# Performance work log

Measured on AMD Instinct MI355X. Metric: run time of the kernel, lower is better.

The kernel has to match this reference:

```python
import jax, jax.numpy as jnp
import numpy as np

VOCAB, HIDDEN, BATCH, EMB, SEQ = 512, 512, 64, 256, 1024


def _lstm_cell(x, h, c, Wih, Whh, bih, bhh):
    # PyTorch LSTMCell gate order: i, f, g, o
    gates = x @ Wih.T + bih + h @ Whh.T + bhh  # [B, 4H]
    i, f, g, o = jnp.split(gates, 4, axis=-1)
    i = jax.nn.sigmoid(i)
    f = jax.nn.sigmoid(f)
    g = jnp.tanh(g)
    o = jax.nn.sigmoid(o)
    c_new = f * c + i * g
    h_new = o * jnp.tanh(c_new)
    return h_new, c_new


def setup_inputs() -> dict:
    key = jax.random.key(0)
    ks = jax.random.split(key, 12)
    s_e = 1.0 / np.sqrt(HIDDEN)
    inp = {
        "x": jax.random.randint(ks[0], (SEQ, BATCH), 0, VOCAB, dtype=jnp.int64)
        if jax.config.jax_enable_x64 else jax.random.randint(ks[0], (SEQ, BATCH), 0, VOCAB, dtype=jnp.int32),
        "h0": jnp.zeros((BATCH, HIDDEN), jnp.float32),
        "c0": jnp.zeros((BATCH, HIDDEN), jnp.float32),
        "emb": jax.random.normal(ks[1], (VOCAB, EMB), jnp.float32),
        "Wih1": jax.random.uniform(ks[2], (4 * HIDDEN, EMB), jnp.float32, -s_e, s_e),
        "Whh1": jax.random.uniform(ks[3], (4 * HIDDEN, HIDDEN), jnp.float32, -s_e, s_e),
        "bih1": jax.random.uniform(ks[4], (4 * HIDDEN,), jnp.float32, -s_e, s_e),
        "bhh1": jax.random.uniform(ks[5], (4 * HIDDEN,), jnp.float32, -s_e, s_e),
        "Wih2": jax.random.uniform(ks[6], (4 * HIDDEN, HIDDEN), jnp.float32, -s_e, s_e),
        "Whh2": jax.random.uniform(ks[7], (4 * HIDDEN, HIDDEN), jnp.float32, -s_e, s_e),
        "bih2": jax.random.uniform(ks[8], (4 * HIDDEN,), jnp.float32, -s_e, s_e),
        "bhh2": jax.random.uniform(ks[9], (4 * HIDDEN,), jnp.float32, -s_e, s_e),
        "Wfc": jax.random.uniform(ks[10], (VOCAB, HIDDEN), jnp.float32, -s_e, s_e),
        "bfc": jax.random.uniform(ks[11], (VOCAB,), jnp.float32, -s_e, s_e),
    }
    return inp


def reference(x, h0, c0, emb, Wih1, Whh1, bih1, bhh1, Wih2, Whh2, bih2, bhh2, Wfc, bfc):
    # Embedding lookup for the whole sequence: [S, B, E]
    x_emb = emb[x]

    def step(carry, xt):
        h1, c1, h2, c2 = carry
        h1, c1 = _lstm_cell(xt, h1, c1, Wih1, Whh1, bih1, bhh1)
        h2, c2 = _lstm_cell(h1, h2, c2, Wih2, Whh2, bih2, bhh2)
        return (h1, c1, h2, c2), h2

    # Both layers start from the same (h0, c0), matching the original hc1, hc2 = (hc, hc)
    _, h2_seq = jax.lax.scan(step, (h0, c0, h0, c0), x_emb)  # [S, B, H]
    # Dropout is identity in eval mode; output projection over all timesteps at once.
    out = jnp.einsum('sbh,vh->sbv', h2_seq, Wfc) + bfc  # [S, B, V]
    return out
```

## Files before the change

kernel.cpp:

```cpp
#include <hip/hip_runtime.h>

#define SEQn   1024
#define BATCHn 64
#define EMBn   256
#define HIDn   512
#define VOCn   512

#define NL1 64
#define NL2 64
#define NFC 16
#define NBLK (NL1 + NL2 + NFC)
#define NPHASE (SEQn + 2)
#define HBUF (BATCHn * HIDn)

using f16   = _Float16;
using half8 = __attribute__((ext_vector_type(8))) _Float16;
using f32x4 = __attribute__((ext_vector_type(4))) float;
using i32x4 = __attribute__((ext_vector_type(4))) int;

#define WS_FLG 0
#define WS_H1  4096
#define WS_H2  (WS_H1 + 8 * HBUF * 2)
#define WS_P1  (WS_H2 + 8 * HBUF * 2)


__device__ __forceinline__ float sigm_(float v) { return 1.0f / (1.0f + __expf(-v)); }
__device__ __forceinline__ float tanh_(float v) { return 1.0f - 2.0f / (__expf(2.0f * v) + 1.0f); }

__device__ __forceinline__ void st_u32_sc1(f16* p, unsigned v) {
  asm volatile("global_store_dword %0, %1, off sc1" :: "v"(p), "v"(v) : "memory");
}
__device__ __forceinline__ void st_b128_sc1(f16* p, f32x4 v) {
  asm volatile("global_store_dwordx4 %0, %1, off sc1" :: "v"(p), "v"(v) : "memory");
}
__device__ __forceinline__ unsigned pack2(float a, float b) {
  f16 lo = (f16)a, hi = (f16)b;
  return (unsigned)__builtin_bit_cast(unsigned short, lo)
       | ((unsigned)__builtin_bit_cast(unsigned short, hi) << 16);
}

__device__ __forceinline__ void ld_frag16(const f16* base, half8 (&a)[16]) {
  const f16* b0 = base + 2048;
  const f16* b1 = base + 6144;
  f32x4 t0,t1,t2,t3,t4,t5,t6,t7,t8,t9,t10,t11,t12,t13,t14,t15;
  asm volatile(
    "global_load_dwordx4 %0,  %16, off offset:-4096 sc1\n\t"
    "global_load_dwordx4 %1,  %16, off offset:-3072 sc1\n\t"
    "global_load_dwordx4 %2,  %16, off offset:-2048 sc1\n\t"
    "global_load_dwordx4 %3,  %16, off offset:-1024 sc1\n\t"
    "global_load_dwordx4 %4,  %16, off sc1\n\t"
    "global_load_dwordx4 %5,  %16, off offset:1024 sc1\n\t"
    "global_load_dwordx4 %6,  %16, off offset:2048 sc1\n\t"
    "global_load_dwordx4 %7,  %16, off offset:3072 sc1\n\t"
    "global_load_dwordx4 %8,  %17, off offset:-4096 sc1\n\t"
    "global_load_dwordx4 %9,  %17, off offset:-3072 sc1\n\t"
    "global_load_dwordx4 %10, %17, off offset:-2048 sc1\n\t"
    "global_load_dwordx4 %11, %17, off offset:-1024 sc1\n\t"
    "global_load_dwordx4 %12, %17, off sc1\n\t"
    "global_load_dwordx4 %13, %17, off offset:1024 sc1\n\t"
    "global_load_dwordx4 %14, %17, off offset:2048 sc1\n\t"
    "global_load_dwordx4 %15, %17, off offset:3072 sc1\n\t"
    "s_waitcnt vmcnt(0)"
    : "=&v"(t0),"=&v"(t1),"=&v"(t2),"=&v"(t3),
      "=&v"(t4),"=&v"(t5),"=&v"(t6),"=&v"(t7),
      "=&v"(t8),"=&v"(t9),"=&v"(t10),"=&v"(t11),
      "=&v"(t12),"=&v"(t13),"=&v"(t14),"=&v"(t15)
    : "v"(b0), "v"(b1)
    : "memory");
  a[0]  = __builtin_bit_cast(half8, t0);   a[1]  = __builtin_bit_cast(half8, t1);
  a[2]  = __builtin_bit_cast(half8, t2);   a[3]  = __builtin_bit_cast(half8, t3);
  a[4]  = __builtin_bit_cast(half8, t4);   a[5]  = __builtin_bit_cast(half8, t5);
  a[6]  = __builtin_bit_cast(half8, t6);   a[7]  = __builtin_bit_cast(half8, t7);
  a[8]  = __builtin_bit_cast(half8, t8);   a[9]  = __builtin_bit_cast(half8, t9);
  a[10] = __builtin_bit_cast(half8, t10);  a[11] = __builtin_bit_cast(half8, t11);
  a[12] = __builtin_bit_cast(half8, t12);  a[13] = __builtin_bit_cast(half8, t13);
  a[14] = __builtin_bit_cast(half8, t14);  a[15] = __builtin_bit_cast(half8, t15);
}

__global__ void k_init(const float* __restrict__ h0, char* __restrict__ ws) {
  int i = blockIdx.x * 256 + threadIdx.x;
  f16* h1b = (f16*)(ws + WS_H1);
  f16* h2b = (f16*)(ws + WS_H2);
  int e = i & (HBUF - 1);
  int r = e >> 9, c = e & 511;
  float v = h0[e];
  int t = (((r >> 4) * 16 + (c >> 5)) * 4 + ((c >> 3) & 3)) * 128 + (r & 15) * 8 + (c & 7);
  int b = i & ~(HBUF - 1);
  h1b[b + t] = (f16)v;
  h2b[b + t] = (f16)v;
  if (i < 1024) ((int*)ws)[i] = 0;
}

__global__ void k_p1(const float* __restrict__ emb, const float* __restrict__ Wih1,
                     const float* __restrict__ bih1, const float* __restrict__ bhh1,
                     char* __restrict__ ws) {
  __shared__ float elds[32 * 256];
  int tid = threadIdx.x;
  int vb = blockIdx.x >> 5, gb = blockIdx.x & 31;
  for (int i = tid; i < 32 * 256; i += 256) elds[i] = emb[vb * 32 * 256 + i];
  __syncthreads();
  int gl = tid & 63, vs = tid >> 6;
  int g = gb * 64 + gl;
  float bias = bih1[g] + bhh1[g];
  float acc[8];
#pragma unroll
  for (int r = 0; r < 8; ++r) acc[r] = bias;
  const float* wrow = Wih1 + g * EMBn;
#pragma unroll 4
  for (int e = 0; e < EMBn; ++e) {
    float w = wrow[e];
#pragma unroll
    for (int r = 0; r < 8; ++r) acc[r] += elds[(vs * 8 + r) * 256 + e] * w;
  }
  f16* P1 = (f16*)(ws + WS_P1);
#pragma unroll
  for (int r = 0; r < 8; ++r) P1[(vb * 32 + vs * 8 + r) * 2048 + g] = (f16)acc[r];
}

__global__ void __launch_bounds__(256, 1)
k_lstm(const int* __restrict__ x, const float* __restrict__ c0,
       const float* __restrict__ Whh1,
       const float* __restrict__ Wih2, const float* __restrict__ Whh2,
       const float* __restrict__ bih2, const float* __restrict__ bhh2,
       const float* __restrict__ Wfc, const float* __restrict__ bfc,
       float* __restrict__ out, char* __restrict__ ws)
{
  __shared__ float part[2][64][34];
  __shared__ f16 p1s[VOCn * 32];
  __shared__ alignas(16) f16 hstage[4][16][8];

  f16* h1base = (f16*)(ws + WS_H1);
  f16* h2base = (f16*)(ws + WS_H2);
  const f16* P1 = (const f16*)(ws + WS_P1);

  const int bid = blockIdx.x, tid = threadIdx.x;
  const int lane = tid & 63, wv = tid >> 6;
  const int cc = lane & 15, qq = lane >> 4;
  const int rep = bid & 3;

  half8 bfrA[2][16];
  float cst[4] = {0.f, 0.f, 0.f, 0.f};
  float bias0 = 0.f, bias1 = 0.f;
  int j0 = 0;
  const int khalf = wv >> 1;
  const int mh = wv & 1;

  if (bid < NL1) {
    j0 = bid * 8;
    int g0 = (cc >> 3) * 512 + j0 + (cc & 7);
#pragma unroll
    for (int nt = 0; nt < 2; ++nt) {
      const float* wr = Whh1 + (g0 + nt * 1024) * HIDn;
#pragma unroll
      for (int ks = 0; ks < 16; ++ks) {
        const float* s = wr + ks * 32 + qq * 8;
        half8 hv;
#pragma unroll
        for (int j = 0; j < 8; ++j) hv[j] = (f16)s[j];
        bfrA[nt][ks] = hv;
      }
    }
    for (int i = tid; i < VOCn * 32; i += 256) {
      int v = i >> 5, n = i & 31;
      p1s[i] = P1[v * 2048 + (n >> 3) * 512 + j0 + (n & 7)];
    }
    if (cc < 8) {
#pragma unroll
      for (int r = 0; r < 4; ++r)
        cst[r] = c0[(wv * 16 + qq * 4 + r) * HIDn + j0 + cc];
    }
  } else if (bid < NL1 + NL2) {
    j0 = (bid - NL1) * 8;
    int g0 = (cc >> 3) * 512 + j0 + (cc & 7);
    const float* W = khalf ? Whh2 : Wih2;
#pragma unroll
    for (int nt = 0; nt < 2; ++nt) {
      const float* wr = W + (g0 + nt * 1024) * HIDn;
#pragma unroll
      for (int ks = 0; ks < 16; ++ks) {
        const float* s = wr + ks * 32 + qq * 8;
        half8 hv;
#pragma unroll
        for (int j = 0; j < 8; ++j) hv[j] = (f16)s[j];
        bfrA[nt][ks] = hv;
      }
    }
    if (khalf == 0) {
      int gc0 = g0, gc1 = g0 + 1024;
      bias0 = bih2[gc0] + bhh2[gc0];
      bias1 = bih2[gc1] + bhh2[gc1];
    }
    {
      int m = tid >> 2, u = tid & 3;
      cst[0] = c0[m * HIDn + j0 + 2 * u];
      cst[1] = c0[m * HIDn + j0 + 2 * u + 1];
    }
  } else {
    j0 = (bid - NL1 - NL2) * 32;
#pragma unroll
    for (int nt = 0; nt < 2; ++nt) {
      const float* wr = Wfc + (j0 + nt * 16 + cc) * HIDn;
#pragma unroll
      for (int ks = 0; ks < 16; ++ks) {
        const float* s = wr + ks * 32 + qq * 8;
        half8 hv;
#pragma unroll
        for (int j = 0; j < 8; ++j) hv[j] = (f16)s[j];
        bfrA[nt][ks] = hv;
      }
    }
    bias0 = bfc[j0 + cc];
    bias1 = bfc[j0 + 16 + cc];
  }
  const int ksJ = (j0 >> 5), qqJ = (j0 >> 3) & 3;
  __syncthreads();

  f32x4 pg0, pg1;
  if (bid < NL1) {
#pragma unroll
    for (int r = 0; r < 4; ++r) {
      int xv = x[wv * 16 + qq * 4 + r];
      pg0[r] = (float)p1s[xv * 32 + cc];
      pg1[r] = (float)p1s[xv * 32 + 16 + cc];
    }
  }

  for (int p = 1; p <= NPHASE; ++p) {
    if (bid < NL1) {
      if (p <= SEQn) {
        const f16* hp = h1base + (rep * 2 + ((p - 1) & 1)) * HBUF;
        f32x4 acc0 = pg0, acc1 = pg1;
        half8 a[16];
        ld_frag16(hp + wv * 8192 + lane * 8, a);
#pragma unroll
        for (int ks = 0; ks < 16; ++ks) {
          acc0 = __builtin_amdgcn_mfma_f32_16x16x32_f16(a[ks], bfrA[0][ks], acc0, 0, 0, 0);
          acc1 = __builtin_amdgcn_mfma_f32_16x16x32_f16(a[ks], bfrA[1][ks], acc1, 0, 0, 0);
        }
        float hv4[4];
#pragma unroll
        for (int r = 0; r < 4; ++r) {
          float fv = __shfl_xor(acc0[r], 8);
          float ov = __shfl_xor(acc1[r], 8);
          float iv = sigm_(acc0[r]);
          float gv = tanh_(acc1[r]);
          float ff = sigm_(fv);
          float oo = sigm_(ov);
          float cn = ff * cst[r] + iv * gv;
          cst[r] = cn;
          hv4[r] = oo * tanh_(cn);
        }
        if (cc < 8) {
#pragma unroll
          for (int r = 0; r < 4; ++r)
            hstage[wv][qq * 4 + r][cc] = (f16)hv4[r];
        }
        __syncthreads();
        {
          f32x4 w = *(const f32x4*)&hstage[lane >> 4][lane & 15][0];
          f16* dst = h1base + (wv * 2 + (p & 1)) * HBUF
                   + (lane >> 4) * 8192 + ksJ * 512 + qqJ * 128 + (lane & 15) * 8;
          st_b128_sc1(dst, w);
        }
      }
    } else if (bid < NL1 + NL2) {
      if (p >= 2 && p <= SEQn + 1) {
        const f16* src = (khalf == 0)
            ? h1base + (rep * 2 + ((p - 1) & 1)) * HBUF
            : h2base + (rep * 2 + (p & 1)) * HBUF;
        f32x4 acc[2][2];
#pragma unroll
        for (int mt = 0; mt < 2; ++mt)
#pragma unroll
          for (int r = 0; r < 4; ++r) {
            acc[mt][0][r] = (khalf == 0) ? bias0 : 0.f;
            acc[mt][1][r] = (khalf == 0) ? bias1 : 0.f;
          }
#pragma unroll
        for (int mt = 0; mt < 2; ++mt) {
          half8 a[16];
          ld_frag16(src + (mh * 2 + mt) * 8192 + lane * 8, a);
#pragma unroll
          for (int ks = 0; ks < 16; ++ks) {
            acc[mt][0] = __builtin_amdgcn_mfma_f32_16x16x32_f16(a[ks], bfrA[0][ks], acc[mt][0], 0, 0, 0);
            acc[mt][1] = __builtin_amdgcn_mfma_f32_16x16x32_f16(a[ks], bfrA[1][ks], acc[mt][1], 0, 0, 0);
          }
        }
#pragma unroll
        for (int mt = 0; mt < 2; ++mt)
#pragma unroll
          for (int nt = 0; nt < 2; ++nt)
#pragma unroll
            for (int r = 0; r < 4; ++r)
              part[khalf][mh * 32 + mt * 16 + qq * 4 + r][nt * 16 + cc] = acc[mt][nt][r];
        __syncthreads();
        {
          int m = tid >> 2, u = tid & 3;
          f16* ho = h2base + ((p - 1) & 1) * HBUF;
          float hh[2];
#pragma unroll
          for (int w2 = 0; w2 < 2; ++w2) {
            int w = 2 * u + w2;
            float gi = part[0][m][w]      + part[1][m][w];
            float gf = part[0][m][8 + w]  + part[1][m][8 + w];
            float gg = part[0][m][16 + w] + part[1][m][16 + w];
            float go = part[0][m][24 + w] + part[1][m][24 + w];
            float cn = sigm_(gf) * cst[w2] + sigm_(gi) * tanh_(gg);
            cst[w2] = cn;
            hh[w2] = sigm_(go) * tanh_(cn);
          }
          unsigned u32v = pack2(hh[0], hh[1]);
          int off = wv * 8192 + ksJ * 512 + qqJ * 128 + lane * 2;
#pragma unroll
          for (int rp = 0; rp < 4; ++rp)
            st_u32_sc1(ho + rp * 2 * HBUF + off, u32v);
        }
      }
    } else {
      if (p >= 3) {
        const f16* h2p = h2base + (rep * 2 + (p & 1)) * HBUF;
        float* op = out + (size_t)(p - 3) * (BATCHn * VOCn);
        half8 a[16];
        ld_frag16(h2p + wv * 8192 + lane * 8, a);
        f32x4 acc0, acc1;
#pragma unroll
        for (int r = 0; r < 4; ++r) { acc0[r] = bias0; acc1[r] = bias1; }
#pragma unroll
        for (int ks = 0; ks < 16; ++ks) {
          acc0 = __builtin_amdgcn_mfma_f32_16x16x32_f16(a[ks], bfrA[0][ks], acc0, 0, 0, 0);
          acc1 = __builtin_amdgcn_mfma_f32_16x16x32_f16(a[ks], bfrA[1][ks], acc1, 0, 0, 0);
        }
#pragma unroll
        for (int r = 0; r < 4; ++r) {
          int m = wv * 16 + qq * 4 + r;
          __builtin_nontemporal_store(acc0[r], &op[m * VOCn + j0 + cc]);
          __builtin_nontemporal_store(acc1[r], &op[m * VOCn + j0 + 16 + cc]);
        }
      }
    }

    if (bid < NL1 + NL2) asm volatile("s_waitcnt vmcnt(0)" ::: "memory");
    __syncthreads();
    if (tid == 0)
      asm volatile("global_store_dword %0, %1, off sc1"
                   :: "v"((int*)ws + bid), "v"(p) : "memory");
    if (bid < NL1 && p < SEQn) {
#pragma unroll
      for (int r = 0; r < 4; ++r) {
        int xv = x[p * 64 + wv * 16 + qq * 4 + r];
        pg0[r] = (float)p1s[xv * 32 + cc];
        pg1[r] = (float)p1s[xv * 32 + 16 + cc];
      }
    }
    if (wv == 0) {
      const int* fp = (const int*)ws + (lane << 2);
      for (;;) {
        i32x4 f;
        asm volatile("global_load_dwordx4 %0, %1, off sc1\n\ts_waitcnt vmcnt(0)"
                     : "=v"(f) : "v"(fp) : "memory");
        int ok = (lane >= 36) ||
                 ((f[0] >= p) & (f[1] >= p) & (f[2] >= p) & (f[3] >= p));
        if (__all(ok)) break;
        __builtin_amdgcn_s_sleep(2);
      }
    }
    __syncthreads();
  }
}

extern "C" void kernel_launch(void* const* d_in, const int* in_sizes, int n_in,
                              void* d_out, int out_size, void* d_ws, size_t ws_size,
                              hipStream_t stream) {
  (void)in_sizes; (void)n_in; (void)out_size; (void)ws_size;
  const int*   x    = (const int*)  d_in[0];
  const float* h0   = (const float*)d_in[1];
  const float* c0   = (const float*)d_in[2];
  const float* emb  = (const float*)d_in[3];
  const float* Wih1 = (const float*)d_in[4];
  const float* Whh1 = (const float*)d_in[5];
  const float* bih1 = (const float*)d_in[6];
  const float* bhh1 = (const float*)d_in[7];
  const float* Wih2 = (const float*)d_in[8];
  const float* Whh2 = (const float*)d_in[9];
  const float* bih2 = (const float*)d_in[10];
  const float* bhh2 = (const float*)d_in[11];
  const float* Wfc  = (const float*)d_in[12];
  const float* bfc  = (const float*)d_in[13];
  char* ws = (char*)d_ws;

  hipLaunchKernelGGL(k_init, dim3(1024), dim3(256), 0, stream, h0, ws);
  hipLaunchKernelGGL(k_p1,   dim3(512), dim3(256), 0, stream, emb, Wih1, bih1, bhh1, ws);
  hipLaunchKernelGGL(k_lstm, dim3(NBLK), dim3(256), 0, stream,
                     x, c0, Whh1, Wih2, Whh2, bih2, bhh2, Wfc, bfc,
                     (float*)d_out, ws);
}
```

Measured before the change: 5.754 ms.

## Halve block count by giving each block sixteen hidden units per layer

Each layer-1, layer-2 and FC block now handles twice as many output columns (16 hidden units, 64 vocab), so the grid falls from 144 to 72 blocks. Fewer blocks take part in the per-step global flag barrier, which is meant to lower the cost of the per-timestep synchronisation. Layer 1 no longer needs shuffles to gather gates, and layer 2 loads both A tiles at once. In exchange each block does twice the MFMA work, holds twice the weight registers (pressure and spill risk), and uses twice the LDS per step.

```diff
diff --git a/kernel.cpp b/kernel.cpp
--- a/kernel.cpp
+++ b/kernel.cpp
@@ -6,9 +6,9 @@
 #define HIDn   512
 #define VOCn   512
 
-#define NL1 64
-#define NL2 64
-#define NFC 16
+#define NL1 32
+#define NL2 32
+#define NFC 8
 #define NBLK (NL1 + NL2 + NFC)
 #define NPHASE (SEQn + 2)
 #define HBUF (BATCHn * HIDn)
@@ -17,6 +17,7 @@
 using half8 = __attribute__((ext_vector_type(8))) _Float16;
 using f32x4 = __attribute__((ext_vector_type(4))) float;
 using i32x4 = __attribute__((ext_vector_type(4))) int;
+using i32x2 = __attribute__((ext_vector_type(2))) int;
 
 #define WS_FLG 0
 #define WS_H1  4096
@@ -29,6 +30,9 @@
 
 __device__ __forceinline__ void st_u32_sc1(f16* p, unsigned v) {
   asm volatile("global_store_dword %0, %1, off sc1" :: "v"(p), "v"(v) : "memory");
+}
+__device__ __forceinline__ void st_b64_sc1(f16* p, i32x2 v) {
+  asm volatile("global_store_dwordx2 %0, %1, off sc1" :: "v"(p), "v"(v) : "memory");
 }
 __device__ __forceinline__ void st_b128_sc1(f16* p, f32x4 v) {
   asm volatile("global_store_dwordx4 %0, %1, off sc1" :: "v"(p), "v"(v) : "memory");
@@ -77,6 +81,74 @@
   a[14] = __builtin_bit_cast(half8, t14);  a[15] = __builtin_bit_cast(half8, t15);
 }
 
+__device__ __forceinline__ void ld_frag32(const f16* baseA, const f16* baseB,
+                                          half8 (&a)[16], half8 (&b)[16]) {
+  const f16* a0 = baseA + 2048;  const f16* a1 = baseA + 6144;
+  const f16* c0p = baseB + 2048; const f16* c1 = baseB + 6144;
+  f32x4 t0,t1,t2,t3,t4,t5,t6,t7,t8,t9,t10,t11,t12,t13,t14,t15;
+  f32x4 u0,u1,u2,u3,u4,u5,u6,u7,u8,u9,u10,u11,u12,u13,u14,u15;
+  asm volatile(
+    "global_load_dwordx4 %0,  %32, off offset:-4096 sc1\n\t"
+    "global_load_dwordx4 %1,  %32, off offset:-3072 sc1\n\t"
+    "global_load_dwordx4 %2,  %32, off offset:-2048 sc1\n\t"
+    "global_load_dwordx4 %3,  %32, off offset:-1024 sc1\n\t"
+    "global_load_dwordx4 %4,  %32, off sc1\n\t"
+    "global_load_dwordx4 %5,  %32, off offset:1024 sc1\n\t"
+    "global_load_dwordx4 %6,  %32, off offset:2048 sc1\n\t"
+    "global_load_dwordx4 %7,  %32, off offset:3072 sc1\n\t"
+    "global_load_dwordx4 %8,  %33, off offset:-4096 sc1\n\t"
+    "global_load_dwordx4 %9,  %33, off offset:-3072 sc1\n\t"
+    "global_load_dwordx4 %10, %33, off offset:-2048 sc1\n\t"
+    "global_load_dwordx4 %11, %33, off offset:-1024 sc1\n\t"
+    "global_load_dwordx4 %12, %33, off sc1\n\t"
+    "global_load_dwordx4 %13, %33, off offset:1024 sc1\n\t"
+    "global_load_dwordx4 %14, %33, off offset:2048 sc1\n\t"
+    "global_load_dwordx4 %15, %33, off offset:3072 sc1\n\t"
+    "global_load_dwordx4 %16, %34, off offset:-4096 sc1\n\t"
+    "global_load_dwordx4 %17, %34, off offset:-3072 sc1\n\t"
+    "global_load_dwordx4 %18, %34, off offset:-2048 sc1\n\t"
+    "global_load_dwordx4 %19, %34, off offset:-1024 sc1\n\t"
+    "global_load_dwordx4 %20, %34, off sc1\n\t"
+    "global_load_dwordx4 %21, %34, off offset:1024 sc1\n\t"
+    "global_load_dwordx4 %22, %34, off offset:2048 sc1\n\t"
+    "global_load_dwordx4 %23, %34, off offset:3072 sc1\n\t"
+    "global_load_dwordx4 %24, %35, off offset:-4096 sc1\n\t"
+    "global_load_dwordx4 %25, %35, off offset:-3072 sc1\n\t"
+    "global_load_dwordx4 %26, %35, off offset:-2048 sc1\n\t"
+    "global_load_dwordx4 %27, %35, off offset:-1024 sc1\n\t"
+    "global_load_dwordx4 %28, %35, off sc1\n\t"
+    "global_load_dwordx4 %29, %35, off offset:1024 sc1\n\t"
+    "global_load_dwordx4 %30, %35, off offset:2048 sc1\n\t"
+    "global_load_dwordx4 %31, %35, off offset:3072 sc1\n\t"
+    "s_waitcnt vmcnt(0)"
+    : "=&v"(t0),"=&v"(t1),"=&v"(t2),"=&v"(t3),
+      "=&v"(t4),"=&v"(t5),"=&v"(t6),"=&v"(t7),
+      "=&v"(t8),"=&v"(t9),"=&v"(t10),"=&v"(t11),
+      "=&v"(t12),"=&v"(t13),"=&v"(t14),"=&v"(t15),
+      "=&v"(u0),"=&v"(u1),"=&v"(u2),"=&v"(u3),
+      "=&v"(u4),"=&v"(u5),"=&v"(u6),"=&v"(u7),
+      "=&v"(u8),"=&v"(u9),"=&v"(u10),"=&v"(u11),
+      "=&v"(u12),"=&v"(u13),"=&v"(u14),"=&v"(u15)
+    : "v"(a0), "v"(a1), "v"(c0p), "v"(c1)
+    : "memory");
+  a[0]  = __builtin_bit_cast(half8, t0);   a[1]  = __builtin_bit_cast(half8, t1);
+  a[2]  = __builtin_bit_cast(half8, t2);   a[3]  = __builtin_bit_cast(half8, t3);
+  a[4]  = __builtin_bit_cast(half8, t4);   a[5]  = __builtin_bit_cast(half8, t5);
+  a[6]  = __builtin_bit_cast(half8, t6);   a[7]  = __builtin_bit_cast(half8, t7);
+  a[8]  = __builtin_bit_cast(half8, t8);   a[9]  = __builtin_bit_cast(half8, t9);
+  a[10] = __builtin_bit_cast(half8, t10);  a[11] = __builtin_bit_cast(half8, t11);
+  a[12] = __builtin_bit_cast(half8, t12);  a[13] = __builtin_bit_cast(half8, t13);
+  a[14] = __builtin_bit_cast(half8, t14);  a[15] = __builtin_bit_cast(half8, t15);
+  b[0]  = __builtin_bit_cast(half8, u0);   b[1]  = __builtin_bit_cast(half8, u1);
+  b[2]  = __builtin_bit_cast(half8, u2);   b[3]  = __builtin_bit_cast(half8, u3);
+  b[4]  = __builtin_bit_cast(half8, u4);   b[5]  = __builtin_bit_cast(half8, u5);
+  b[6]  = __builtin_bit_cast(half8, u6);   b[7]  = __builtin_bit_cast(half8, u7);
+  b[8]  = __builtin_bit_cast(half8, u8);   b[9]  = __builtin_bit_cast(half8, u9);
+  b[10] = __builtin_bit_cast(half8, u10);  b[11] = __builtin_bit_cast(half8, u11);
+  b[12] = __builtin_bit_cast(half8, u12);  b[13] = __builtin_bit_cast(half8, u13);
+  b[14] = __builtin_bit_cast(half8, u14);  b[15] = __builtin_bit_cast(half8, u15);
+}
+
 __global__ void k_init(const float* __restrict__ h0, char* __restrict__ ws) {
   int i = blockIdx.x * 256 + threadIdx.x;
   f16* h1b = (f16*)(ws + WS_H1);
@@ -125,9 +197,9 @@
        const float* __restrict__ Wfc, const float* __restrict__ bfc,
        float* __restrict__ out, char* __restrict__ ws)
 {
-  __shared__ float part[2][64][34];
-  __shared__ f16 p1s[VOCn * 32];
-  __shared__ alignas(16) f16 hstage[4][16][8];
+  __shared__ float part[2][64][68];
+  __shared__ f16 p1s[VOCn * 64];
+  __shared__ alignas(16) f16 hstage[4][2][16][8];
 
   f16* h1base = (f16*)(ws + WS_H1);
   f16* h2base = (f16*)(ws + WS_H2);
@@ -138,19 +210,18 @@
   const int cc = lane & 15, qq = lane >> 4;
   const int rep = bid & 3;
 
-  half8 bfrA[2][16];
+  half8 bfrA[4][16];
   float cst[4] = {0.f, 0.f, 0.f, 0.f};
-  float bias0 = 0.f, bias1 = 0.f;
+  float bias[4] = {0.f, 0.f, 0.f, 0.f};
   int j0 = 0;
   const int khalf = wv >> 1;
   const int mh = wv & 1;
 
   if (bid < NL1) {
-    j0 = bid * 8;
-    int g0 = (cc >> 3) * 512 + j0 + (cc & 7);
-#pragma unroll
-    for (int nt = 0; nt < 2; ++nt) {
-      const float* wr = Whh1 + (g0 + nt * 1024) * HIDn;
+    j0 = bid * 16;
+#pragma unroll
+    for (int nt = 0; nt < 4; ++nt) {
+      const float* wr = Whh1 + (nt * 512 + j0 + cc) * HIDn;
 #pragma unroll
       for (int ks = 0; ks < 16; ++ks) {
         const float* s = wr + ks * 32 + qq * 8;
@@ -160,22 +231,19 @@
         bfrA[nt][ks] = hv;
       }
     }
-    for (int i = tid; i < VOCn * 32; i += 256) {
-      int v = i >> 5, n = i & 31;
-      p1s[i] = P1[v * 2048 + (n >> 3) * 512 + j0 + (n & 7)];
-    }
-    if (cc < 8) {
-#pragma unroll
-      for (int r = 0; r < 4; ++r)
-        cst[r] = c0[(wv * 16 + qq * 4 + r) * HIDn + j0 + cc];
-    }
+    for (int i = tid; i < VOCn * 64; i += 256) {
+      int v = i >> 6, n = i & 63;
+      p1s[i] = P1[v * 2048 + (n >> 4) * 512 + j0 + (n & 15)];
+    }
+#pragma unroll
+    for (int r = 0; r < 4; ++r)
+      cst[r] = c0[(wv * 16 + qq * 4 + r) * HIDn + j0 + cc];
   } else if (bid < NL1 + NL2) {
-    j0 = (bid - NL1) * 8;
-    int g0 = (cc >> 3) * 512 + j0 + (cc & 7);
+    j0 = (bid - NL1) * 16;
     const float* W = khalf ? Whh2 : Wih2;
 #pragma unroll
-    for (int nt = 0; nt < 2; ++nt) {
-      const float* wr = W + (g0 + nt * 1024) * HIDn;
+    for (int nt = 0; nt < 4; ++nt) {
+      const float* wr = W + (nt * 512 + j0 + cc) * HIDn;
 #pragma unroll
       for (int ks = 0; ks < 16; ++ks) {
         const float* s = wr + ks * 32 + qq * 8;
@@ -186,19 +254,22 @@
       }
     }
     if (khalf == 0) {
-      int gc0 = g0, gc1 = g0 + 1024;
-      bias0 = bih2[gc0] + bhh2[gc0];
-      bias1 = bih2[gc1] + bhh2[gc1];
+#pragma unroll
+      for (int nt = 0; nt < 4; ++nt) {
+        int g = nt * 512 + j0 + cc;
+        bias[nt] = bih2[g] + bhh2[g];
+      }
     }
     {
-      int m = tid >> 2, u = tid & 3;
-      cst[0] = c0[m * HIDn + j0 + 2 * u];
-      cst[1] = c0[m * HIDn + j0 + 2 * u + 1];
+      int m = tid >> 2, us = (tid & 3) * 4;
+#pragma unroll
+      for (int w2 = 0; w2 < 4; ++w2)
+        cst[w2] = c0[m * HIDn + j0 + us + w2];
     }
   } else {
-    j0 = (bid - NL1 - NL2) * 32;
-#pragma unroll
-    for (int nt = 0; nt < 2; ++nt) {
+    j0 = (bid - NL1 - NL2) * 64;
+#pragma unroll
+    for (int nt = 0; nt < 4; ++nt) {
       const float* wr = Wfc + (j0 + nt * 16 + cc) * HIDn;
 #pragma unroll
       for (int ks = 0; ks < 16; ++ks) {
@@ -208,20 +279,20 @@
         for (int j = 0; j < 8; ++j) hv[j] = (f16)s[j];
         bfrA[nt][ks] = hv;
       }
-    }
-    bias0 = bfc[j0 + cc];
-    bias1 = bfc[j0 + 16 + cc];
+      bias[nt] = bfc[j0 + nt * 16 + cc];
+    }
   }
   const int ksJ = (j0 >> 5), qqJ = (j0 >> 3) & 3;
   __syncthreads();
 
-  f32x4 pg0, pg1;
+  f32x4 pg[4];
   if (bid < NL1) {
 #pragma unroll
     for (int r = 0; r < 4; ++r) {
       int xv = x[wv * 16 + qq * 4 + r];
-      pg0[r] = (float)p1s[xv * 32 + cc];
-      pg1[r] = (float)p1s[xv * 32 + 16 + cc];
+#pragma unroll
+      for (int t = 0; t < 4; ++t)
+        pg[t][r] = (float)p1s[xv * 64 + t * 16 + cc];
     }
   }
 
@@ -229,38 +300,39 @@
     if (bid < NL1) {
       if (p <= SEQn) {
         const f16* hp = h1base + (rep * 2 + ((p - 1) & 1)) * HBUF;
-        f32x4 acc0 = pg0, acc1 = pg1;
+        f32x4 acc[4];
+#pragma unroll
+        for (int t = 0; t < 4; ++t) acc[t] = pg[t];
         half8 a[16];
         ld_frag16(hp + wv * 8192 + lane * 8, a);
 #pragma unroll
         for (int ks = 0; ks < 16; ++ks) {
-          acc0 = __builtin_amdgcn_mfma_f32_16x16x32_f16(a[ks], bfrA[0][ks], acc0, 0, 0, 0);
-          acc1 = __builtin_amdgcn_mfma_f32_16x16x32_f16(a[ks], bfrA[1][ks], acc1, 0, 0, 0);
+#pragma unroll
+          for (int t = 0; t < 4; ++t)
+            acc[t] = __builtin_amdgcn_mfma_f32_16x16x32_f16(a[ks], bfrA[t][ks], acc[t], 0, 0, 0);
         }
         float hv4[4];
 #pragma unroll
         for (int r = 0; r < 4; ++r) {
-          float fv = __shfl_xor(acc0[r], 8);
-          float ov = __shfl_xor(acc1[r], 8);
-          float iv = sigm_(acc0[r]);
-          float gv = tanh_(acc1[r]);
-          float ff = sigm_(fv);
-          float oo = sigm_(ov);
+          float iv = sigm_(acc[0][r]);
+          float ff = sigm_(acc[1][r]);
+          float gv = tanh_(acc[2][r]);
+          float oo = sigm_(acc[3][r]);
           float cn = ff * cst[r] + iv * gv;
           cst[r] = cn;
           hv4[r] = oo * tanh_(cn);
         }
-        if (cc < 8) {
-#pragma unroll
-          for (int r = 0; r < 4; ++r)
-            hstage[wv][qq * 4 + r][cc] = (f16)hv4[r];
-        }
+#pragma unroll
+        for (int r = 0; r < 4; ++r)
+          hstage[wv][cc >> 3][qq * 4 + r][cc & 7] = (f16)hv4[r];
         __syncthreads();
         {
-          f32x4 w = *(const f32x4*)&hstage[lane >> 4][lane & 15][0];
-          f16* dst = h1base + (wv * 2 + (p & 1)) * HBUF
-                   + (lane >> 4) * 8192 + ksJ * 512 + qqJ * 128 + (lane & 15) * 8;
-          st_b128_sc1(dst, w);
+          int tp = tid & 127, rp0 = tid >> 7;
+          f32x4 w = ((const f32x4*)hstage)[tp];
+          int mb = tp >> 5, uh = (tp >> 4) & 1, r15 = tp & 15;
+          int dst16 = mb * 8192 + ksJ * 512 + (qqJ + uh) * 128 + r15 * 8;
+          st_b128_sc1(h1base + (rp0 * 2 + (p & 1)) * HBUF + dst16, w);
+          st_b128_sc1(h1base + ((rp0 + 2) * 2 + (p & 1)) * HBUF + dst16, w);
         }
       }
     } else if (bid < NL1 + NL2) {
@@ -268,52 +340,55 @@
         const f16* src = (khalf == 0)
             ? h1base + (rep * 2 + ((p - 1) & 1)) * HBUF
             : h2base + (rep * 2 + (p & 1)) * HBUF;
-        f32x4 acc[2][2];
+        half8 a0[16], a1[16];
+        ld_frag32(src + (mh * 2 + 0) * 8192 + lane * 8,
+                  src + (mh * 2 + 1) * 8192 + lane * 8, a0, a1);
+        f32x4 acc[2][4];
 #pragma unroll
         for (int mt = 0; mt < 2; ++mt)
 #pragma unroll
-          for (int r = 0; r < 4; ++r) {
-            acc[mt][0][r] = (khalf == 0) ? bias0 : 0.f;
-            acc[mt][1][r] = (khalf == 0) ? bias1 : 0.f;
+          for (int nt = 0; nt < 4; ++nt)
+#pragma unroll
+            for (int r = 0; r < 4; ++r)
+              acc[mt][nt][r] = (khalf == 0) ? bias[nt] : 0.f;
+#pragma unroll
+        for (int ks = 0; ks < 16; ++ks) {
+#pragma unroll
+          for (int nt = 0; nt < 4; ++nt) {
+            acc[0][nt] = __builtin_amdgcn_mfma_f32_16x16x32_f16(a0[ks], bfrA[nt][ks], acc[0][nt], 0, 0, 0);
+            acc[1][nt] = __builtin_amdgcn_mfma_f32_16x16x32_f16(a1[ks], bfrA[nt][ks], acc[1][nt], 0, 0, 0);
           }
-#pragma unroll
-        for (int mt = 0; mt < 2; ++mt) {
-          half8 a[16];
-          ld_frag16(src + (mh * 2 + mt) * 8192 + lane * 8, a);
-#pragma unroll
-          for (int ks = 0; ks < 16; ++ks) {
-            acc[mt][0] = __builtin_amdgcn_mfma_f32_16x16x32_f16(a[ks], bfrA[0][ks], acc[mt][0], 0, 0, 0);
-            acc[mt][1] = __builtin_amdgcn_mfma_f32_16x16x32_f16(a[ks], bfrA[1][ks], acc[mt][1], 0, 0, 0);
-          }
         }
 #pragma unroll
         for (int mt = 0; mt < 2; ++mt)
 #pragma unroll
-          for (int nt = 0; nt < 2; ++nt)
+          for (int nt = 0; nt < 4; ++nt)
 #pragma unroll
             for (int r = 0; r < 4; ++r)
               part[khalf][mh * 32 + mt * 16 + qq * 4 + r][nt * 16 + cc] = acc[mt][nt][r];
         __syncthreads();
         {
-          int m = tid >> 2, u = tid & 3;
+          int m = tid >> 2, us = (tid & 3) * 4;
           f16* ho = h2base + ((p - 1) & 1) * HBUF;
-          float hh[2];
-#pragma unroll
-          for (int w2 = 0; w2 < 2; ++w2) {
-            int w = 2 * u + w2;
-            float gi = part[0][m][w]      + part[1][m][w];
-            float gf = part[0][m][8 + w]  + part[1][m][8 + w];
-            float gg = part[0][m][16 + w] + part[1][m][16 + w];
-            float go = part[0][m][24 + w] + part[1][m][24 + w];
-            float cn = sigm_(gf) * cst[w2] + sigm_(gi) * tanh_(gg);
+          f32x4 gi = *(const f32x4*)&part[0][m][us]      + *(const f32x4*)&part[1][m][us];
+          f32x4 gf = *(const f32x4*)&part[0][m][16 + us] + *(const f32x4*)&part[1][m][16 + us];
+          f32x4 gg = *(const f32x4*)&part[0][m][32 + us] + *(const f32x4*)&part[1][m][32 + us];
+          f32x4 go = *(const f32x4*)&part[0][m][48 + us] + *(const f32x4*)&part[1][m][48 + us];
+          float hh[4];
+#pragma unroll
+          for (int w2 = 0; w2 < 4; ++w2) {
+            float cn = sigm_(gf[w2]) * cst[w2] + sigm_(gi[w2]) * tanh_(gg[w2]);
             cst[w2] = cn;
-            hh[w2] = sigm_(go) * tanh_(cn);
+            hh[w2] = sigm_(go[w2]) * tanh_(cn);
           }
-          unsigned u32v = pack2(hh[0], hh[1]);
-          int off = wv * 8192 + ksJ * 512 + qqJ * 128 + lane * 2;
+          i32x2 v;
+          v[0] = (int)pack2(hh[0], hh[1]);
+          v[1] = (int)pack2(hh[2], hh[3]);
+          int off = (m >> 4) * 8192 + ksJ * 512 + (qqJ + (us >> 3)) * 128
+                  + (m & 15) * 8 + (us & 7);
 #pragma unroll
           for (int rp = 0; rp < 4; ++rp)
-            st_u32_sc1(ho + rp * 2 * HBUF + off, u32v);
+            st_b64_sc1(ho + rp * 2 * HBUF + off, v);
         }
       }
     } else {
@@ -322,20 +397,24 @@
         float* op = out + (size_t)(p - 3) * (BATCHn * VOCn);
         half8 a[16];
         ld_frag16(h2p + wv * 8192 + lane * 8, a);
-        f32x4 acc0, acc1;
-#pragma unroll
-        for (int r = 0; r < 4; ++r) { acc0[r] = bias0; acc1[r] = bias1; }
+        f32x4 acc[4];
+#pragma unroll
+        for (int nt = 0; nt < 4; ++nt)
+#pragma unroll
+          for (int r = 0; r < 4; ++r) acc[nt][r] = bias[nt];
 #pragma unroll
         for (int ks = 0; ks < 16; ++ks) {
-          acc0 = __builtin_amdgcn_mfma_f32_16x16x32_f16(a[ks], bfrA[0][ks], acc0, 0, 0, 0);
-          acc1 = __builtin_amdgcn_mfma_f32_16x16x32_f16(a[ks], bfrA[1][ks], acc1, 0, 0, 0);
-        }
-#pragma unroll
-        for (int r = 0; r < 4; ++r) {
-          int m = wv * 16 + qq * 4 + r;
-          __builtin_nontemporal_store(acc0[r], &op[m * VOCn + j0 + cc]);
-          __builtin_nontemporal_store(acc1[r], &op[m * VOCn + j0 + 16 + cc]);
-        }
+#pragma unroll
+          for (int nt = 0; nt < 4; ++nt)
+            acc[nt] = __builtin_amdgcn_mfma_f32_16x16x32_f16(a[ks], bfrA[nt][ks], acc[nt], 0, 0, 0);
+        }
+#pragma unroll
+        for (int nt = 0; nt < 4; ++nt)
+#pragma unroll
+          for (int r = 0; r < 4; ++r) {
+            int m = wv * 16 + qq * 4 + r;
+            __builtin_nontemporal_store(acc[nt][r], &op[m * VOCn + j0 + nt * 16 + cc]);
+          }
       }
     }
 
@@ -348,8 +427,9 @@
 #pragma unroll
       for (int r = 0; r < 4; ++r) {
         int xv = x[p * 64 + wv * 16 + qq * 4 + r];
-        pg0[r] = (float)p1s[xv * 32 + cc];
-        pg1[r] = (float)p1s[xv * 32 + 16 + cc];
+#pragma unroll
+        for (int t = 0; t < 4; ++t)
+          pg[t][r] = (float)p1s[xv * 64 + t * 16 + cc];
       }
     }
     if (wv == 0) {
@@ -358,7 +438,7 @@
         i32x4 f;
         asm volatile("global_load_dwordx4 %0, %1, off sc1\n\ts_waitcnt vmcnt(0)"
                      : "=v"(f) : "v"(fp) : "memory");
-        int ok = (lane >= 36) ||
+        int ok = (lane >= 18) ||
                  ((f[0] >= p) & (f[1] >= p) & (f[2] >= p) & (f[3] >= p));
         if (__all(ok)) break;
         __builtin_amdgcn_s_sleep(2);
```

Result: slower. 6.607 ms (+14.8%).
